# Kernel optimization log

Measured on AMD Instinct MI355X. Metric: run time of the kernel, lower is better.

## Reference

```python
import jax, jax.numpy as jnp
import numpy as np

E, T_MAX, H, L, V = 384, 256, 6, 6, 65
DH = E // H  # 64
EPS = 1e-5


def setup_inputs() -> dict:
    key = jax.random.key(0)
    ks = jax.random.split(key, 24)
    B, T = 128, 256
    s = 0.02
    inp = {
        "input_indices": jax.random.randint(ks[0], (B, T), 0, V, dtype=jnp.int64) if jax.config.read("jax_enable_x64") else jax.random.randint(ks[0], (B, T), 0, V, dtype=jnp.int32),
        "targets": jax.random.randint(ks[1], (B, T), 0, V, dtype=jnp.int32),
        "tok_emb": s * jax.random.normal(ks[2], (V, E), jnp.float32),
        "pos_emb": s * jax.random.normal(ks[3], (T_MAX, E), jnp.float32),
        "Wq": s * jax.random.normal(ks[4], (L, H, E, DH), jnp.float32),
        "Wk": s * jax.random.normal(ks[5], (L, H, E, DH), jnp.float32),
        "Wv": s * jax.random.normal(ks[6], (L, H, E, DH), jnp.float32),
        "Wo": s * jax.random.normal(ks[7], (L, E, E), jnp.float32),
        "bo": jnp.zeros((L, E), jnp.float32),
        "ln1_s": jnp.ones((L, E), jnp.float32),
        "ln1_b": jnp.zeros((L, E), jnp.float32),
        "ln2_s": jnp.ones((L, E), jnp.float32),
        "ln2_b": jnp.zeros((L, E), jnp.float32),
        "W1": s * jax.random.normal(ks[8], (L, E, 4 * E), jnp.float32),
        "b1": jnp.zeros((L, 4 * E), jnp.float32),
        "W2": s * jax.random.normal(ks[9], (L, 4 * E, E), jnp.float32),
        "b2": jnp.zeros((L, E), jnp.float32),
        "lnf_s": jnp.ones((E,), jnp.float32),
        "lnf_b": jnp.zeros((E,), jnp.float32),
        "Wout": s * jax.random.normal(ks[10], (E, V), jnp.float32),
        "bout": jnp.zeros((V,), jnp.float32),
    }
    return inp


def _ln(x, s, b):
    m = x.mean(-1, keepdims=True)
    v = ((x - m) ** 2).mean(-1, keepdims=True)
    return (x - m) * jax.lax.rsqrt(v + EPS) * s + b


def _forward(input_indices, targets, tok_emb, pos_emb, Wq, Wk, Wv, Wo, bo,
             ln1_s, ln1_b, ln2_s, ln2_b, W1, b1, W2, b2, lnf_s, lnf_b, Wout, bout):
    B, T = input_indices.shape
    x = tok_emb[input_indices] + pos_emb[:T]  # [B,T,E]
    causal = jnp.tril(jnp.ones((T, T), bool))
    scale = DH ** -0.5

    def block(x, p):
        wq, wk, wv, wo, bo_, l1s, l1b, l2s, l2b, w1, b1_, w2, b2_ = p
        h = _ln(x, l1s, l1b)
        q = jnp.einsum("bte,hed->bhtd", h, wq)
        k = jnp.einsum("bte,hed->bhtd", h, wk)
        v = jnp.einsum("bte,hed->bhtd", h, wv)
        scores = jnp.einsum("bhtd,bhsd->bhts", q, k) * scale
        scores = jnp.where(causal, scores, -jnp.inf)
        w = jax.nn.softmax(scores, axis=-1)
        att = jnp.einsum("bhts,bhsd->bhtd", w, v)  # [B,H,T,DH]
        att = att.transpose(0, 2, 1, 3).reshape(B, T, E)  # concat heads
        x = x + att @ wo + bo_
        h2 = _ln(x, l2s, l2b)
        ff = jax.nn.relu(h2 @ w1 + b1_) @ w2 + b2_
        return x + ff, None

    x, _ = jax.lax.scan(block, x, (Wq, Wk, Wv, Wo, bo, ln1_s, ln1_b, ln2_s, ln2_b, W1, b1, W2, b2))
    x = _ln(x, lnf_s, lnf_b)
    logits = x @ Wout + bout  # [B,T,V]
    logp = jax.nn.log_softmax(logits, axis=-1)
    nll = -jnp.take_along_axis(logp, targets[..., None], axis=-1)[..., 0]
    loss = nll.mean()
    return logits, loss


def reference(input_indices, targets, tok_emb, pos_emb, Wq, Wk, Wv, Wo, bo,
              ln1_s, ln1_b, ln2_s, ln2_b, W1, b1, W2, b2, lnf_s, lnf_b, Wout, bout):
    return _forward(input_indices, targets, tok_emb, pos_emb, Wq, Wk, Wv, Wo, bo,
                    ln1_s, ln1_b, ln2_s, ln2_b, W1, b1, W2, b2, lnf_s, lnf_b, Wout, bout)
```

## Files before the change

### kernel.cpp

```cpp
#include <hip/hip_runtime.h>

#define BT      32768
#define T_SEQ   256
#define E_DIM   384
#define NH      6
#define NL      6
#define VOC     65
#define FF_DIM  1536
#define QKV_N   1152

typedef short bf16x8 __attribute__((ext_vector_type(8)));
typedef float f32x4  __attribute__((ext_vector_type(4)));
typedef unsigned short u16;

typedef const unsigned int __attribute__((address_space(1))) gu32;
typedef unsigned int       __attribute__((address_space(3))) lu32;

__device__ __forceinline__ u16 f2bf(float x) {
  unsigned u = __builtin_bit_cast(unsigned, x);
  u += 0x7fffu + ((u >> 16) & 1u);
  return (u16)(u >> 16);
}
__device__ __forceinline__ float bf2f(u16 v) {
  unsigned u = ((unsigned)v) << 16;
  return __builtin_bit_cast(float, u);
}

__device__ __forceinline__ void load_lds_16(const void* g, void* l) {
  __builtin_amdgcn_global_load_lds((gu32*)g, (lu32*)l, 16, 0, 0);
}

__global__ __launch_bounds__(256) void transpose_t(
    const float* __restrict__ src, u16* __restrict__ dst, int R, int C,
    long sbs, long dbs_outer, int inner, long dbs_inner, long dbase) {
  __shared__ float t[32][33];
  const int b = blockIdx.z;
  const float* s = src + (long)b * sbs;
  u16* d = dst + dbase + (long)(b / inner) * dbs_outer + (long)(b % inner) * dbs_inner;
  const int r0 = blockIdx.x * 32, c0 = blockIdx.y * 32;
  const int tx = threadIdx.x & 31, ty = threadIdx.x >> 5;
#pragma unroll
  for (int i = 0; i < 4; i++) {
    int rr = ty + i * 8;
    int r = r0 + rr, c = c0 + tx;
    if (r < R && c < C) t[rr][tx] = s[(long)r * C + c];
  }
  __syncthreads();
#pragma unroll
  for (int i = 0; i < 4; i++) {
    int cc = ty + i * 8;
    int c = c0 + cc, r = r0 + tx;
    if (c < C && r < R) d[(long)c * R + r] = f2bf(t[tx][cc]);
  }
}

__global__ __launch_bounds__(256) void embed_k(const int* __restrict__ idx,
                                               const float* __restrict__ tok,
                                               const float* __restrict__ pos,
                                               u16* __restrict__ x) {
  int i = blockIdx.x * 256 + threadIdx.x;
  int bt = i / 48, q = i - bt * 48;
  int t = bt & 255;
  const float4* tp = (const float4*)(tok + (size_t)idx[bt] * E_DIM + q * 8);
  const float4* pp = (const float4*)(pos + (size_t)t * E_DIM + q * 8);
  float4 a0 = tp[0], a1 = tp[1], p0 = pp[0], p1 = pp[1];
  u16 o[8];
  o[0] = f2bf(a0.x + p0.x); o[1] = f2bf(a0.y + p0.y);
  o[2] = f2bf(a0.z + p0.z); o[3] = f2bf(a0.w + p0.w);
  o[4] = f2bf(a1.x + p1.x); o[5] = f2bf(a1.y + p1.y);
  o[6] = f2bf(a1.z + p1.z); o[7] = f2bf(a1.w + p1.w);
  *(bf16x8*)(x + (size_t)bt * E_DIM + q * 8) = *(bf16x8*)o;
}

__global__ __launch_bounds__(256) void ln_k(const u16* __restrict__ x,
                                            const float* __restrict__ gam,
                                            const float* __restrict__ bet,
                                            u16* __restrict__ out) {
  int tid = threadIdx.x, lane = tid & 63, w = tid >> 6;
  size_t token = (size_t)blockIdx.x * 4 + w;
  const u16* xr = x + token * E_DIM;
  u16 raw[6];
  *(uint2*)raw          = *(const uint2*)(xr + 4 * lane);
  *(unsigned*)(raw + 4) = *(const unsigned*)(xr + 256 + 2 * lane);
  float v[6]; float s = 0.f;
#pragma unroll
  for (int i = 0; i < 6; i++) { v[i] = bf2f(raw[i]); s += v[i]; }
#pragma unroll
  for (int d = 1; d < 64; d <<= 1) s += __shfl_xor(s, d);
  float mean = s * (1.f / E_DIM);
  float q = 0.f;
#pragma unroll
  for (int i = 0; i < 6; i++) { float d0 = v[i] - mean; q += d0 * d0; }
#pragma unroll
  for (int d = 1; d < 64; d <<= 1) q += __shfl_xor(q, d);
  float r = rsqrtf(q * (1.f / E_DIM) + 1e-5f);
  int e[6] = {4 * lane, 4 * lane + 1, 4 * lane + 2, 4 * lane + 3,
              256 + 2 * lane, 256 + 2 * lane + 1};
  u16 o[6];
#pragma unroll
  for (int i = 0; i < 6; i++)
    o[i] = f2bf((v[i] - mean) * r * gam[e[i]] + bet[e[i]]);
  u16* orow = out + token * E_DIM;
  *(uint2*)(orow + 4 * lane)        = *(uint2*)o;
  *(unsigned*)(orow + 256 + 2 * lane) = *(unsigned*)(o + 4);
}

__global__ __launch_bounds__(256) void gemm_bt(
    const u16* __restrict__ A, const u16* __restrict__ Bt, int K, int Nstore,
    const float* __restrict__ bias, const u16* __restrict__ resid,
    u16* __restrict__ outH, float* __restrict__ outF, int relu) {
  __shared__ u16 smem[8192];
  u16* As = smem;
  u16* Bs = smem + 4096;
  const int tid = threadIdx.x, lane = tid & 63, wv = tid >> 6;
  const int quad = lane >> 4, l16 = lane & 15;
  const int m0 = blockIdx.x * 128, n0 = blockIdx.y * 128;
  const int wm = (wv & 1) * 64, wn = (wv >> 1) * 64;
  const int srow = lane >> 2, scol = (lane & 3) * 8;

  f32x4 acc[4][4];
#pragma unroll
  for (int i = 0; i < 4; i++)
#pragma unroll
    for (int j = 0; j < 4; j++) acc[i][j] = (f32x4){0.f, 0.f, 0.f, 0.f};

  for (int k0 = 0; k0 < K; k0 += 32) {
    __syncthreads();
#pragma unroll
    for (int j = 0; j < 2; j++) {
      int rid = wv * 2 + j;
      int r = rid * 16 + srow;
      load_lds_16(A  + (size_t)(m0 + r) * K + (k0 + scol), &As[rid * 512]);
      load_lds_16(Bt + (size_t)(n0 + r) * K + (k0 + scol), &Bs[rid * 512]);
    }
    __syncthreads();
    bf16x8 af[4], bfr[4];
#pragma unroll
    for (int i = 0; i < 4; i++) af[i]  = *(const bf16x8*)&As[(wm + i * 16 + l16) * 32 + quad * 8];
#pragma unroll
    for (int j = 0; j < 4; j++) bfr[j] = *(const bf16x8*)&Bs[(wn + j * 16 + l16) * 32 + quad * 8];
#pragma unroll
    for (int i = 0; i < 4; i++)
#pragma unroll
      for (int j = 0; j < 4; j++)
        acc[i][j] = __builtin_amdgcn_mfma_f32_16x16x32_bf16(af[i], bfr[j], acc[i][j], 0, 0, 0);
  }

  if (outH) {
#pragma unroll
    for (int p = 0; p < 4; p++) {
      __syncthreads();
      if ((wv >> 1) == (p >> 1)) {
#pragma unroll
        for (int jj = 0; jj < 2; jj++) {
          int j = (p & 1) * 2 + jj;
          int gn = n0 + wn + j * 16 + l16;
          float bv = bias ? bias[gn] : 0.f;
          int lcol = jj * 16 + l16;
#pragma unroll
          for (int i = 0; i < 4; i++)
#pragma unroll
            for (int r = 0; r < 4; r++) {
              float v = acc[i][j][r] + bv;
              if (relu) v = fmaxf(v, 0.f);
              smem[(wm + i * 16 + quad * 4 + r) * 36 + lcol] = f2bf(v);
            }
        }
      }
      __syncthreads();
      const int gc0 = n0 + p * 32;
#pragma unroll
      for (int s = 0; s < 4; s++) {
        int row = s * 32 + (tid >> 3);
        int seg = (tid & 7) * 4;
        u16 pk[4];
        *(uint2*)pk = *(const uint2*)&smem[row * 36 + seg];
        size_t o = (size_t)(m0 + row) * Nstore + gc0 + seg;
        if (resid) {
          u16 rv[4];
          *(uint2*)rv = *(const uint2*)&resid[o];
#pragma unroll
          for (int q2 = 0; q2 < 4; q2++) pk[q2] = f2bf(bf2f(pk[q2]) + bf2f(rv[q2]));
        }
        *(uint2*)&outH[o] = *(uint2*)pk;
      }
    }
  } else {
#pragma unroll
    for (int j = 0; j < 4; j++) {
      const int gn = n0 + wn + j * 16 + l16;
      if (gn < Nstore) {
        const float bv = bias ? bias[gn] : 0.f;
#pragma unroll
        for (int i = 0; i < 4; i++)
#pragma unroll
          for (int r = 0; r < 4; r++) {
            const int gm = m0 + wm + i * 16 + quad * 4 + r;
            outF[(size_t)gm * Nstore + gn] = acc[i][j][r] + bv;
          }
      }
    }
  }
}

__global__ __launch_bounds__(512) void attn_k(const u16* __restrict__ qkv,
                                              u16* __restrict__ att) {
  __shared__ u16 Kc[64 * 64];
  __shared__ u16 Vtc[64 * 64];
  __shared__ u16 Pl[8 * 32 * 64];
  const int b = blockIdx.x / NH, h = blockIdx.x % NH;
  const int tid = threadIdx.x, lane = tid & 63, w = tid >> 6;
  const int quad = lane >> 4, l16 = lane & 15;
  const int rowb = b * T_SEQ;

  bf16x8 qf[2][2];
#pragma unroll
  for (int mi = 0; mi < 2; mi++)
#pragma unroll
    for (int kk = 0; kk < 2; kk++)
      qf[mi][kk] = *(const bf16x8*)(qkv + (size_t)(rowb + w * 32 + mi * 16 + l16) * QKV_N +
                                    h * 64 + kk * 32 + quad * 8);

  f32x4 Oa[2][4];
  float mrun[2][4], lrun[2][4];
#pragma unroll
  for (int mi = 0; mi < 2; mi++) {
#pragma unroll
    for (int di = 0; di < 4; di++) Oa[mi][di] = (f32x4){0.f, 0.f, 0.f, 0.f};
#pragma unroll
    for (int r = 0; r < 4; r++) { mrun[mi][r] = -1e30f; lrun[mi][r] = 0.f; }
  }

  u16* Pw = &Pl[w * 2048];
  const int nch = (w >> 1) + 1;
  const int sr = tid >> 3, sseg = (tid & 7) * 8;

  for (int c = 0; c < 4; c++) {
    const int s0 = c * 64;
    __syncthreads();
    *(uint4*)&Kc[sr * 64 + sseg] =
        *(const uint4*)(qkv + (size_t)(rowb + s0 + sr) * QKV_N + 384 + h * 64 + sseg);
    {
      union { uint4 u; u16 us[8]; } tb;
      tb.u = *(const uint4*)(qkv + (size_t)(rowb + s0 + sr) * QKV_N + 768 + h * 64 + sseg);
#pragma unroll
      for (int j = 0; j < 8; j++) Vtc[(sseg + j) * 64 + sr] = tb.us[j];
    }
    __syncthreads();
    if (c >= nch) continue;

    f32x4 S[2][4];
    bf16x8 kf[4][2];
#pragma unroll
    for (int ni = 0; ni < 4; ni++)
#pragma unroll
      for (int kk = 0; kk < 2; kk++)
        kf[ni][kk] = *(const bf16x8*)&Kc[(ni * 16 + l16) * 64 + kk * 32 + quad * 8];
#pragma unroll
    for (int mi = 0; mi < 2; mi++)
#pragma unroll
      for (int ni = 0; ni < 4; ni++) {
        f32x4 z = (f32x4){0.f, 0.f, 0.f, 0.f};
        z = __builtin_amdgcn_mfma_f32_16x16x32_bf16(qf[mi][0], kf[ni][0], z, 0, 0, 0);
        S[mi][ni] = __builtin_amdgcn_mfma_f32_16x16x32_bf16(qf[mi][1], kf[ni][1], z, 0, 0, 0);
      }
    const bool diag = (c == nch - 1);
#pragma unroll
    for (int mi = 0; mi < 2; mi++)
#pragma unroll
      for (int ni = 0; ni < 4; ni++)
#pragma unroll
        for (int r = 0; r < 4; r++) {
          float xv = S[mi][ni][r] * 0.125f;
          if (diag) {
            int t = w * 32 + mi * 16 + quad * 4 + r;
            int s = s0 + ni * 16 + l16;
            if (s > t) xv = -1e30f;
          }
          S[mi][ni][r] = xv;
        }
#pragma unroll
    for (int mi = 0; mi < 2; mi++)
#pragma unroll
      for (int r = 0; r < 4; r++) {
        float mx = fmaxf(fmaxf(S[mi][0][r], S[mi][1][r]), fmaxf(S[mi][2][r], S[mi][3][r]));
        mx = fmaxf(mx, __shfl_xor(mx, 1));
        mx = fmaxf(mx, __shfl_xor(mx, 2));
        mx = fmaxf(mx, __shfl_xor(mx, 4));
        mx = fmaxf(mx, __shfl_xor(mx, 8));
        float mnew = fmaxf(mrun[mi][r], mx);
        float alpha = __expf(mrun[mi][r] - mnew);
        float ls = 0.f;
#pragma unroll
        for (int ni = 0; ni < 4; ni++) {
          float p = __expf(S[mi][ni][r] - mnew);
          S[mi][ni][r] = p; ls += p;
        }
        ls += __shfl_xor(ls, 1); ls += __shfl_xor(ls, 2);
        ls += __shfl_xor(ls, 4); ls += __shfl_xor(ls, 8);
        lrun[mi][r] = lrun[mi][r] * alpha + ls;
        mrun[mi][r] = mnew;
#pragma unroll
        for (int di = 0; di < 4; di++) Oa[mi][di][r] *= alpha;
      }
#pragma unroll
    for (int mi = 0; mi < 2; mi++)
#pragma unroll
      for (int ni = 0; ni < 4; ni++)
#pragma unroll
        for (int r = 0; r < 4; r++)
          Pw[(mi * 16 + quad * 4 + r) * 64 + ni * 16 + l16] = f2bf(S[mi][ni][r]);
    bf16x8 pf[2][2], vf[4][2];
#pragma unroll
    for (int mi = 0; mi < 2; mi++)
#pragma unroll
      for (int kk = 0; kk < 2; kk++)
        pf[mi][kk] = *(const bf16x8*)&Pw[(mi * 16 + l16) * 64 + kk * 32 + quad * 8];
#pragma unroll
    for (int di = 0; di < 4; di++)
#pragma unroll
      for (int kk = 0; kk < 2; kk++)
        vf[di][kk] = *(const bf16x8*)&Vtc[(di * 16 + l16) * 64 + kk * 32 + quad * 8];
#pragma unroll
    for (int mi = 0; mi < 2; mi++)
#pragma unroll
      for (int di = 0; di < 4; di++) {
        Oa[mi][di] = __builtin_amdgcn_mfma_f32_16x16x32_bf16(pf[mi][0], vf[di][0], Oa[mi][di], 0, 0, 0);
        Oa[mi][di] = __builtin_amdgcn_mfma_f32_16x16x32_bf16(pf[mi][1], vf[di][1], Oa[mi][di], 0, 0, 0);
      }
  }

#pragma unroll
  for (int mi = 0; mi < 2; mi++)
#pragma unroll
    for (int r = 0; r < 4; r++) {
      float inv = 1.f / lrun[mi][r];
      int t = w * 32 + mi * 16 + quad * 4 + r;
#pragma unroll
      for (int di = 0; di < 4; di++)
        att[(size_t)(rowb + t) * E_DIM + h * 64 + di * 16 + l16] = f2bf(Oa[mi][di][r] * inv);
    }
}

__global__ __launch_bounds__(256) void loss_k(const float* __restrict__ logits,
                                              const int* __restrict__ tgt,
                                              float* __restrict__ loss) {
  __shared__ float part[4];
  const int tid = threadIdx.x, lane = tid & 63, w = tid >> 6;
  const int wave_id = blockIdx.x * 4 + w;
  float acc = 0.f;
  for (int t = wave_id; t < BT; t += 2048) {
    const float* row = logits + (size_t)t * VOC;
    float a = row[lane];
    float b = (lane == 0) ? row[64] : -1e30f;
    float mx = fmaxf(a, b);
#pragma unroll
    for (int d = 1; d < 64; d <<= 1) mx = fmaxf(mx, __shfl_xor(mx, d));
    float sum = __expf(a - mx) + ((lane == 0) ? __expf(b - mx) : 0.f);
#pragma unroll
    for (int d = 1; d < 64; d <<= 1) sum += __shfl_xor(sum, d);
    if (lane == 0) acc += mx + __logf(sum) - row[tgt[t]];
  }
  if (lane == 0) part[w] = acc;
  __syncthreads();
  if (tid == 0)
    atomicAdd(loss, (part[0] + part[1] + part[2] + part[3]) * (1.f / (float)BT));
}

extern "C" void kernel_launch(void* const* d_in, const int* in_sizes, int n_in,
                              void* d_out, int out_size, void* d_ws, size_t ws_size,
                              hipStream_t stream) {
  (void)in_sizes; (void)n_in; (void)out_size; (void)ws_size;
  const int*   idx  = (const int*)d_in[0];
  const int*   tgt  = (const int*)d_in[1];
  const float* tok  = (const float*)d_in[2];
  const float* pos  = (const float*)d_in[3];
  const float* Wq   = (const float*)d_in[4];
  const float* Wk   = (const float*)d_in[5];
  const float* Wv   = (const float*)d_in[6];
  const float* Wo   = (const float*)d_in[7];
  const float* bo   = (const float*)d_in[8];
  const float* ln1s = (const float*)d_in[9];
  const float* ln1b = (const float*)d_in[10];
  const float* ln2s = (const float*)d_in[11];
  const float* ln2b = (const float*)d_in[12];
  const float* W1   = (const float*)d_in[13];
  const float* b1   = (const float*)d_in[14];
  const float* W2   = (const float*)d_in[15];
  const float* b2   = (const float*)d_in[16];
  const float* lnfs = (const float*)d_in[17];
  const float* lnfb = (const float*)d_in[18];
  const float* Wout = (const float*)d_in[19];
  const float* bout = (const float*)d_in[20];

  char* w = (char*)d_ws;
  u16* x      = (u16*)w;    w += (size_t)BT * E_DIM * 2;
  u16* hb     = (u16*)w;    w += (size_t)BT * E_DIM * 2;
  u16* attb   = (u16*)w;    w += (size_t)BT * E_DIM * 2;
  u16* big    = (u16*)w;    w += (size_t)BT * FF_DIM * 2;
  u16* Wqkv_t = (u16*)w;    w += (size_t)NL * QKV_N * E_DIM * 2;
  u16* Wo_t   = (u16*)w;    w += (size_t)NL * E_DIM * E_DIM * 2;
  u16* W1_t   = (u16*)w;    w += (size_t)NL * FF_DIM * E_DIM * 2;
  u16* W2_t   = (u16*)w;    w += (size_t)NL * E_DIM * FF_DIM * 2;
  u16* Wout_t = (u16*)w;    w += (size_t)128 * E_DIM * 2;
  u16* qkv = big;
  u16* ff  = big;

  float* logits = (float*)d_out;
  float* loss   = logits + (size_t)BT * VOC;

  hipMemsetAsync(Wout_t, 0, 128 * E_DIM * 2, stream);
  transpose_t<<<dim3(12, 2, 36), 256, 0, stream>>>(Wq, Wqkv_t, 384, 64,
      24576, 442368, 6, 24576, 0);
  transpose_t<<<dim3(12, 2, 36), 256, 0, stream>>>(Wk, Wqkv_t, 384, 64,
      24576, 442368, 6, 24576, (long)384 * 384);
  transpose_t<<<dim3(12, 2, 36), 256, 0, stream>>>(Wv, Wqkv_t, 384, 64,
      24576, 442368, 6, 24576, (long)768 * 384);
  transpose_t<<<dim3(12, 12, 6), 256, 0, stream>>>(Wo, Wo_t, 384, 384,
      147456, 147456, 1, 0, 0);
  transpose_t<<<dim3(12, 48, 6), 256, 0, stream>>>(W1, W1_t, 384, 1536,
      589824, 589824, 1, 0, 0);
  transpose_t<<<dim3(48, 12, 6), 256, 0, stream>>>(W2, W2_t, 1536, 384,
      589824, 589824, 1, 0, 0);
  transpose_t<<<dim3(12, 3, 1), 256, 0, stream>>>(Wout, Wout_t, 384, 65,
      0, 0, 1, 0, 0);

  embed_k<<<6144, 256, 0, stream>>>(idx, tok, pos, x);

  for (int l = 0; l < NL; l++) {
    ln_k<<<8192, 256, 0, stream>>>(x, ln1s + l * E_DIM, ln1b + l * E_DIM, hb);
    gemm_bt<<<dim3(256, 9), 256, 0, stream>>>(hb, Wqkv_t + (size_t)l * QKV_N * E_DIM,
                                              384, QKV_N, nullptr, nullptr, qkv, nullptr, 0);
    attn_k<<<768, 512, 0, stream>>>(qkv, attb);
    gemm_bt<<<dim3(256, 3), 256, 0, stream>>>(attb, Wo_t + (size_t)l * E_DIM * E_DIM,
                                              384, E_DIM, bo + l * E_DIM, x, x, nullptr, 0);
    ln_k<<<8192, 256, 0, stream>>>(x, ln2s + l * E_DIM, ln2b + l * E_DIM, hb);
    gemm_bt<<<dim3(256, 12), 256, 0, stream>>>(hb, W1_t + (size_t)l * FF_DIM * E_DIM,
                                               384, FF_DIM, b1 + l * FF_DIM, nullptr, ff, nullptr, 1);
    gemm_bt<<<dim3(256, 3), 256, 0, stream>>>(ff, W2_t + (size_t)l * E_DIM * FF_DIM,
                                              1536, E_DIM, b2 + l * E_DIM, x, x, nullptr, 0);
  }
  ln_k<<<8192, 256, 0, stream>>>(x, lnfs, lnfb, hb);
  gemm_bt<<<dim3(256, 1), 256, 0, stream>>>(hb, Wout_t, 384, VOC, bout, nullptr, nullptr, logits, 0);

  hipMemsetAsync(loss, 0, 4, stream);
  loss_k<<<512, 256, 0, stream>>>(logits, tgt, loss);
}
```

Before: 1.912 ms.

## Double-buffer GEMM LDS tiles and use 256-row tiles for wide GEMMs

The GEMM kernel becomes a template on the M tile size and double-buffers its A/B LDS tiles, so the global-to-LDS load for the next K step is issued before the MFMAs on the current step. This removes one of the two barriers per K iteration. The QKV and FF1 GEMMs switch to 256-row tiles, which halves the number of blocks and gives more reuse of each B tile. The cost is more LDS (up to 48 KB) and more accumulator registers per block, and launch bounds are set to keep 2-3 blocks per CU.

```diff
diff --git a/kernel.cpp b/kernel.cpp
--- a/kernel.cpp
+++ b/kernel.cpp
@@ -101,55 +101,73 @@
   for (int i = 0; i < 6; i++)
     o[i] = f2bf((v[i] - mean) * r * gam[e[i]] + bet[e[i]]);
   u16* orow = out + token * E_DIM;
-  *(uint2*)(orow + 4 * lane)        = *(uint2*)o;
+  *(uint2*)(orow + 4 * lane)          = *(uint2*)o;
   *(unsigned*)(orow + 256 + 2 * lane) = *(unsigned*)(o + 4);
 }
 
-__global__ __launch_bounds__(256) void gemm_bt(
+template<int TM>
+__global__ __launch_bounds__(256, TM == 256 ? 2 : 3) void gemm_bt(
     const u16* __restrict__ A, const u16* __restrict__ Bt, int K, int Nstore,
     const float* __restrict__ bias, const u16* __restrict__ resid,
     u16* __restrict__ outH, float* __restrict__ outF, int relu) {
-  __shared__ u16 smem[8192];
+  constexpr int MI = TM / 32;
+  __shared__ u16 smem[TM * 64 + 8192];
   u16* As = smem;
-  u16* Bs = smem + 4096;
+  u16* Bs = smem + TM * 64;
   const int tid = threadIdx.x, lane = tid & 63, wv = tid >> 6;
   const int quad = lane >> 4, l16 = lane & 15;
-  const int m0 = blockIdx.x * 128, n0 = blockIdx.y * 128;
-  const int wm = (wv & 1) * 64, wn = (wv >> 1) * 64;
+  const int m0 = blockIdx.x * TM, n0 = blockIdx.y * 128;
+  const int wm = (wv & 1) * (TM / 2), wn = (wv >> 1) * 64;
   const int srow = lane >> 2, scol = (lane & 3) * 8;
 
-  f32x4 acc[4][4];
-#pragma unroll
-  for (int i = 0; i < 4; i++)
+  f32x4 acc[MI][4];
+#pragma unroll
+  for (int i = 0; i < MI; i++)
 #pragma unroll
     for (int j = 0; j < 4; j++) acc[i][j] = (f32x4){0.f, 0.f, 0.f, 0.f};
 
-  for (int k0 = 0; k0 < K; k0 += 32) {
-    __syncthreads();
+  auto stage = [&](int sel, int k0) {
+    u16* Ab = As + sel * (TM * 32);
+    u16* Bb = Bs + sel * 4096;
+#pragma unroll
+    for (int j = 0; j < TM / 64; j++) {
+      int rid = wv * (TM / 64) + j;
+      int r = rid * 16 + srow;
+      load_lds_16(A + (size_t)(m0 + r) * K + (k0 + scol), Ab + rid * 512);
+    }
 #pragma unroll
     for (int j = 0; j < 2; j++) {
       int rid = wv * 2 + j;
       int r = rid * 16 + srow;
-      load_lds_16(A  + (size_t)(m0 + r) * K + (k0 + scol), &As[rid * 512]);
-      load_lds_16(Bt + (size_t)(n0 + r) * K + (k0 + scol), &Bs[rid * 512]);
-    }
-    __syncthreads();
-    bf16x8 af[4], bfr[4];
-#pragma unroll
-    for (int i = 0; i < 4; i++) af[i]  = *(const bf16x8*)&As[(wm + i * 16 + l16) * 32 + quad * 8];
-#pragma unroll
-    for (int j = 0; j < 4; j++) bfr[j] = *(const bf16x8*)&Bs[(wn + j * 16 + l16) * 32 + quad * 8];
-#pragma unroll
-    for (int i = 0; i < 4; i++)
+      load_lds_16(Bt + (size_t)(n0 + r) * K + (k0 + scol), Bb + rid * 512);
+    }
+  };
+
+  const int NK = K >> 5;
+  stage(0, 0);
+  __syncthreads();
+  for (int kt = 0; kt < NK; kt++) {
+    const int cur = kt & 1;
+    if (kt + 1 < NK) stage(cur ^ 1, (kt + 1) * 32);
+    const u16* Ab = As + cur * (TM * 32);
+    const u16* Bb = Bs + cur * 4096;
+    bf16x8 af[MI], bfr[4];
+#pragma unroll
+    for (int i = 0; i < MI; i++) af[i]  = *(const bf16x8*)&Ab[(wm + i * 16 + l16) * 32 + quad * 8];
+#pragma unroll
+    for (int j = 0; j < 4; j++)  bfr[j] = *(const bf16x8*)&Bb[(wn + j * 16 + l16) * 32 + quad * 8];
+#pragma unroll
+    for (int i = 0; i < MI; i++)
 #pragma unroll
       for (int j = 0; j < 4; j++)
         acc[i][j] = __builtin_amdgcn_mfma_f32_16x16x32_bf16(af[i], bfr[j], acc[i][j], 0, 0, 0);
+    __syncthreads();
   }
 
   if (outH) {
 #pragma unroll
     for (int p = 0; p < 4; p++) {
-      __syncthreads();
+      if (p) __syncthreads();
       if ((wv >> 1) == (p >> 1)) {
 #pragma unroll
         for (int jj = 0; jj < 2; jj++) {
@@ -158,7 +176,7 @@
           float bv = bias ? bias[gn] : 0.f;
           int lcol = jj * 16 + l16;
 #pragma unroll
-          for (int i = 0; i < 4; i++)
+          for (int i = 0; i < MI; i++)
 #pragma unroll
             for (int r = 0; r < 4; r++) {
               float v = acc[i][j][r] + bv;
@@ -170,7 +188,7 @@
       __syncthreads();
       const int gc0 = n0 + p * 32;
 #pragma unroll
-      for (int s = 0; s < 4; s++) {
+      for (int s = 0; s < TM / 32; s++) {
         int row = s * 32 + (tid >> 3);
         int seg = (tid & 7) * 4;
         u16 pk[4];
@@ -192,7 +210,7 @@
       if (gn < Nstore) {
         const float bv = bias ? bias[gn] : 0.f;
 #pragma unroll
-        for (int i = 0; i < 4; i++)
+        for (int i = 0; i < MI; i++)
 #pragma unroll
           for (int r = 0; r < 4; r++) {
             const int gm = m0 + wm + i * 16 + quad * 4 + r;
@@ -429,19 +447,19 @@
 
   for (int l = 0; l < NL; l++) {
     ln_k<<<8192, 256, 0, stream>>>(x, ln1s + l * E_DIM, ln1b + l * E_DIM, hb);
-    gemm_bt<<<dim3(256, 9), 256, 0, stream>>>(hb, Wqkv_t + (size_t)l * QKV_N * E_DIM,
-                                              384, QKV_N, nullptr, nullptr, qkv, nullptr, 0);
+    gemm_bt<256><<<dim3(128, 9), 256, 0, stream>>>(hb, Wqkv_t + (size_t)l * QKV_N * E_DIM,
+                                                   384, QKV_N, nullptr, nullptr, qkv, nullptr, 0);
     attn_k<<<768, 512, 0, stream>>>(qkv, attb);
-    gemm_bt<<<dim3(256, 3), 256, 0, stream>>>(attb, Wo_t + (size_t)l * E_DIM * E_DIM,
-                                              384, E_DIM, bo + l * E_DIM, x, x, nullptr, 0);
+    gemm_bt<128><<<dim3(256, 3), 256, 0, stream>>>(attb, Wo_t + (size_t)l * E_DIM * E_DIM,
+                                                   384, E_DIM, bo + l * E_DIM, x, x, nullptr, 0);
     ln_k<<<8192, 256, 0, stream>>>(x, ln2s + l * E_DIM, ln2b + l * E_DIM, hb);
-    gemm_bt<<<dim3(256, 12), 256, 0, stream>>>(hb, W1_t + (size_t)l * FF_DIM * E_DIM,
-                                               384, FF_DIM, b1 + l * FF_DIM, nullptr, ff, nullptr, 1);
-    gemm_bt<<<dim3(256, 3), 256, 0, stream>>>(ff, W2_t + (size_t)l * E_DIM * FF_DIM,
-                                              1536, E_DIM, b2 + l * E_DIM, x, x, nullptr, 0);
+    gemm_bt<256><<<dim3(128, 12), 256, 0, stream>>>(hb, W1_t + (size_t)l * FF_DIM * E_DIM,
+                                                    384, FF_DIM, b1 + l * FF_DIM, nullptr, ff, nullptr, 1);
+    gemm_bt<128><<<dim3(256, 3), 256, 0, stream>>>(ff, W2_t + (size_t)l * E_DIM * FF_DIM,
+                                                   1536, E_DIM, b2 + l * E_DIM, x, x, nullptr, 0);
   }
   ln_k<<<8192, 256, 0, stream>>>(x, lnfs, lnfb, hb);
-  gemm_bt<<<dim3(256, 1), 256, 0, stream>>>(hb, Wout_t, 384, VOC, bout, nullptr, nullptr, logits, 0);
+  gemm_bt<128><<<dim3(256, 1), 256, 0, stream>>>(hb, Wout_t, 384, VOC, bout, nullptr, nullptr, logits, 0);
 
   hipMemsetAsync(loss, 0, 4, stream);
   loss_k<<<512, 256, 0, stream>>>(logits, tgt, loss);
```

Measured after the change: 1.866 ms. 1.02x faster.

## Load GEMM operands directly from global into registers with double buffering

Applied to the files above, without the earlier changes.

Replaces the shared-memory staged GEMM, which used global_load_lds with two barriers per K-step, by a version where each wave loads its MFMA fragments straight from global memory into registers. Two register buffers hold alternating K-halves so loads overlap the MFMAs. The epilogue becomes per-wave, using a private LDS tile with 16-byte stores and no block-wide barriers. This removes cross-wave data sharing, so each wave refetches A and B rows through cache. The fragment-shaped global loads are also less coalesced.

```diff
diff --git a/kernel.cpp b/kernel.cpp
--- a/kernel.cpp
+++ b/kernel.cpp
@@ -13,9 +13,6 @@
 typedef float f32x4  __attribute__((ext_vector_type(4)));
 typedef unsigned short u16;
 
-typedef const unsigned int __attribute__((address_space(1))) gu32;
-typedef unsigned int       __attribute__((address_space(3))) lu32;
-
 __device__ __forceinline__ u16 f2bf(float x) {
   unsigned u = __builtin_bit_cast(unsigned, x);
   u += 0x7fffu + ((u >> 16) & 1u);
@@ -24,10 +21,6 @@
 __device__ __forceinline__ float bf2f(u16 v) {
   unsigned u = ((unsigned)v) << 16;
   return __builtin_bit_cast(float, u);
-}
-
-__device__ __forceinline__ void load_lds_16(const void* g, void* l) {
-  __builtin_amdgcn_global_load_lds((gu32*)g, (lu32*)l, 16, 0, 0);
 }
 
 __global__ __launch_bounds__(256) void transpose_t(
@@ -101,22 +94,21 @@
   for (int i = 0; i < 6; i++)
     o[i] = f2bf((v[i] - mean) * r * gam[e[i]] + bet[e[i]]);
   u16* orow = out + token * E_DIM;
-  *(uint2*)(orow + 4 * lane)        = *(uint2*)o;
+  *(uint2*)(orow + 4 * lane)          = *(uint2*)o;
   *(unsigned*)(orow + 256 + 2 * lane) = *(unsigned*)(o + 4);
 }
 
-__global__ __launch_bounds__(256) void gemm_bt(
+__global__ __launch_bounds__(256) void gemm_nb(
     const u16* __restrict__ A, const u16* __restrict__ Bt, int K, int Nstore,
     const float* __restrict__ bias, const u16* __restrict__ resid,
     u16* __restrict__ outH, float* __restrict__ outF, int relu) {
-  __shared__ u16 smem[8192];
-  u16* As = smem;
-  u16* Bs = smem + 4096;
+  __shared__ u16 cb[4][64 * 68];
   const int tid = threadIdx.x, lane = tid & 63, wv = tid >> 6;
   const int quad = lane >> 4, l16 = lane & 15;
-  const int m0 = blockIdx.x * 128, n0 = blockIdx.y * 128;
-  const int wm = (wv & 1) * 64, wn = (wv >> 1) * 64;
-  const int srow = lane >> 2, scol = (lane & 3) * 8;
+  const int m0 = blockIdx.x * 128 + (wv & 1) * 64;
+  const int n0 = blockIdx.y * 128 + (wv >> 1) * 64;
+  const u16* Ap = A  + (size_t)(m0 + l16) * K + quad * 8;
+  const u16* Bp = Bt + (size_t)(n0 + l16) * K + quad * 8;
 
   f32x4 acc[4][4];
 #pragma unroll
@@ -124,78 +116,76 @@
 #pragma unroll
     for (int j = 0; j < 4; j++) acc[i][j] = (f32x4){0.f, 0.f, 0.f, 0.f};
 
-  for (int k0 = 0; k0 < K; k0 += 32) {
-    __syncthreads();
-#pragma unroll
-    for (int j = 0; j < 2; j++) {
-      int rid = wv * 2 + j;
-      int r = rid * 16 + srow;
-      load_lds_16(A  + (size_t)(m0 + r) * K + (k0 + scol), &As[rid * 512]);
-      load_lds_16(Bt + (size_t)(n0 + r) * K + (k0 + scol), &Bs[rid * 512]);
-    }
-    __syncthreads();
-    bf16x8 af[4], bfr[4];
-#pragma unroll
-    for (int i = 0; i < 4; i++) af[i]  = *(const bf16x8*)&As[(wm + i * 16 + l16) * 32 + quad * 8];
-#pragma unroll
-    for (int j = 0; j < 4; j++) bfr[j] = *(const bf16x8*)&Bs[(wn + j * 16 + l16) * 32 + quad * 8];
+  bf16x8 a0[4], b0[4], a1[4], b1[4];
+#pragma unroll
+  for (int i = 0; i < 4; i++) a0[i] = *(const bf16x8*)(Ap + (size_t)(i * 16) * K);
+#pragma unroll
+  for (int j = 0; j < 4; j++) b0[j] = *(const bf16x8*)(Bp + (size_t)(j * 16) * K);
+
+  for (int k0 = 0; k0 < K; k0 += 64) {
+#pragma unroll
+    for (int i = 0; i < 4; i++) a1[i] = *(const bf16x8*)(Ap + (size_t)(i * 16) * K + k0 + 32);
+#pragma unroll
+    for (int j = 0; j < 4; j++) b1[j] = *(const bf16x8*)(Bp + (size_t)(j * 16) * K + k0 + 32);
 #pragma unroll
     for (int i = 0; i < 4; i++)
 #pragma unroll
       for (int j = 0; j < 4; j++)
-        acc[i][j] = __builtin_amdgcn_mfma_f32_16x16x32_bf16(af[i], bfr[j], acc[i][j], 0, 0, 0);
+        acc[i][j] = __builtin_amdgcn_mfma_f32_16x16x32_bf16(a0[i], b0[j], acc[i][j], 0, 0, 0);
+    if (k0 + 64 < K) {
+#pragma unroll
+      for (int i = 0; i < 4; i++) a0[i] = *(const bf16x8*)(Ap + (size_t)(i * 16) * K + k0 + 64);
+#pragma unroll
+      for (int j = 0; j < 4; j++) b0[j] = *(const bf16x8*)(Bp + (size_t)(j * 16) * K + k0 + 64);
+    }
+#pragma unroll
+    for (int i = 0; i < 4; i++)
+#pragma unroll
+      for (int j = 0; j < 4; j++)
+        acc[i][j] = __builtin_amdgcn_mfma_f32_16x16x32_bf16(a1[i], b1[j], acc[i][j], 0, 0, 0);
   }
 
   if (outH) {
-#pragma unroll
-    for (int p = 0; p < 4; p++) {
-      __syncthreads();
-      if ((wv >> 1) == (p >> 1)) {
-#pragma unroll
-        for (int jj = 0; jj < 2; jj++) {
-          int j = (p & 1) * 2 + jj;
-          int gn = n0 + wn + j * 16 + l16;
-          float bv = bias ? bias[gn] : 0.f;
-          int lcol = jj * 16 + l16;
-#pragma unroll
-          for (int i = 0; i < 4; i++)
-#pragma unroll
-            for (int r = 0; r < 4; r++) {
-              float v = acc[i][j][r] + bv;
-              if (relu) v = fmaxf(v, 0.f);
-              smem[(wm + i * 16 + quad * 4 + r) * 36 + lcol] = f2bf(v);
-            }
+    u16* L = cb[wv];
+#pragma unroll
+    for (int j = 0; j < 4; j++) {
+      int gn = n0 + j * 16 + l16;
+      float bv = bias ? bias[gn] : 0.f;
+#pragma unroll
+      for (int i = 0; i < 4; i++)
+#pragma unroll
+        for (int r = 0; r < 4; r++) {
+          float v = acc[i][j][r] + bv;
+          if (relu) v = fmaxf(v, 0.f);
+          L[(i * 16 + quad * 4 + r) * 68 + j * 16 + l16] = f2bf(v);
         }
+    }
+    const int sr = lane >> 3, seg = (lane & 7) * 8;
+#pragma unroll
+    for (int s = 0; s < 8; s++) {
+      int row = s * 8 + sr;
+      u16 pk[8];
+      *(uint4*)pk = *(const uint4*)&L[row * 68 + seg];
+      size_t o = (size_t)(m0 + row) * Nstore + n0 + seg;
+      if (resid) {
+        u16 rv[8];
+        *(uint4*)rv = *(const uint4*)&resid[o];
+#pragma unroll
+        for (int q2 = 0; q2 < 8; q2++) pk[q2] = f2bf(bf2f(pk[q2]) + bf2f(rv[q2]));
       }
-      __syncthreads();
-      const int gc0 = n0 + p * 32;
-#pragma unroll
-      for (int s = 0; s < 4; s++) {
-        int row = s * 32 + (tid >> 3);
-        int seg = (tid & 7) * 4;
-        u16 pk[4];
-        *(uint2*)pk = *(const uint2*)&smem[row * 36 + seg];
-        size_t o = (size_t)(m0 + row) * Nstore + gc0 + seg;
-        if (resid) {
-          u16 rv[4];
-          *(uint2*)rv = *(const uint2*)&resid[o];
-#pragma unroll
-          for (int q2 = 0; q2 < 4; q2++) pk[q2] = f2bf(bf2f(pk[q2]) + bf2f(rv[q2]));
-        }
-        *(uint2*)&outH[o] = *(uint2*)pk;
-      }
+      *(uint4*)&outH[o] = *(uint4*)pk;
     }
   } else {
 #pragma unroll
     for (int j = 0; j < 4; j++) {
-      const int gn = n0 + wn + j * 16 + l16;
+      const int gn = n0 + j * 16 + l16;
       if (gn < Nstore) {
         const float bv = bias ? bias[gn] : 0.f;
 #pragma unroll
         for (int i = 0; i < 4; i++)
 #pragma unroll
           for (int r = 0; r < 4; r++) {
-            const int gm = m0 + wm + i * 16 + quad * 4 + r;
+            const int gm = m0 + i * 16 + quad * 4 + r;
             outF[(size_t)gm * Nstore + gn] = acc[i][j][r] + bv;
           }
       }
@@ -429,19 +419,19 @@
 
   for (int l = 0; l < NL; l++) {
     ln_k<<<8192, 256, 0, stream>>>(x, ln1s + l * E_DIM, ln1b + l * E_DIM, hb);
-    gemm_bt<<<dim3(256, 9), 256, 0, stream>>>(hb, Wqkv_t + (size_t)l * QKV_N * E_DIM,
+    gemm_nb<<<dim3(256, 9), 256, 0, stream>>>(hb, Wqkv_t + (size_t)l * QKV_N * E_DIM,
                                               384, QKV_N, nullptr, nullptr, qkv, nullptr, 0);
     attn_k<<<768, 512, 0, stream>>>(qkv, attb);
-    gemm_bt<<<dim3(256, 3), 256, 0, stream>>>(attb, Wo_t + (size_t)l * E_DIM * E_DIM,
+    gemm_nb<<<dim3(256, 3), 256, 0, stream>>>(attb, Wo_t + (size_t)l * E_DIM * E_DIM,
                                               384, E_DIM, bo + l * E_DIM, x, x, nullptr, 0);
     ln_k<<<8192, 256, 0, stream>>>(x, ln2s + l * E_DIM, ln2b + l * E_DIM, hb);
-    gemm_bt<<<dim3(256, 12), 256, 0, stream>>>(hb, W1_t + (size_t)l * FF_DIM * E_DIM,
+    gemm_nb<<<dim3(256, 12), 256, 0, stream>>>(hb, W1_t + (size_t)l * FF_DIM * E_DIM,
                                                384, FF_DIM, b1 + l * FF_DIM, nullptr, ff, nullptr, 1);
-    gemm_bt<<<dim3(256, 3), 256, 0, stream>>>(ff, W2_t + (size_t)l * E_DIM * FF_DIM,
+    gemm_nb<<<dim3(256, 3), 256, 0, stream>>>(ff, W2_t + (size_t)l * E_DIM * FF_DIM,
                                               1536, E_DIM, b2 + l * E_DIM, x, x, nullptr, 0);
   }
   ln_k<<<8192, 256, 0, stream>>>(x, lnfs, lnfb, hb);
-  gemm_bt<<<dim3(256, 1), 256, 0, stream>>>(hb, Wout_t, 384, VOC, bout, nullptr, nullptr, logits, 0);
+  gemm_nb<<<dim3(256, 1), 256, 0, stream>>>(hb, Wout_t, 384, VOC, bout, nullptr, nullptr, logits, 0);
 
   hipMemsetAsync(loss, 0, 4, stream);
   loss_k<<<512, 256, 0, stream>>>(logits, tgt, loss);
```

Result: slower. 3.087 ms (+61.4%).

## Double-buffer GEMM tiles via register prefetch with padded LDS rows

Applied to the files above, without the earlier changes.

Replaces the direct global-to-LDS loads in the GEMM with register-staged prefetching two k-tiles ahead into double-buffered shared memory, using a single barrier per iteration. LDS rows are padded to 34 elements to reduce bank conflicts on fragment reads. The aim is to overlap global memory latency with MFMA work and remove one barrier per k-step. In exchange it uses more registers and twice the LDS, which may lower occupancy, and the 34-element stride leaves the 16-byte vector accesses only 4-byte aligned.

```diff
diff --git a/kernel.cpp b/kernel.cpp
--- a/kernel.cpp
+++ b/kernel.cpp
@@ -13,9 +13,6 @@
 typedef float f32x4  __attribute__((ext_vector_type(4)));
 typedef unsigned short u16;
 
-typedef const unsigned int __attribute__((address_space(1))) gu32;
-typedef unsigned int       __attribute__((address_space(3))) lu32;
-
 __device__ __forceinline__ u16 f2bf(float x) {
   unsigned u = __builtin_bit_cast(unsigned, x);
   u += 0x7fffu + ((u >> 16) & 1u);
@@ -26,8 +23,8 @@
   return __builtin_bit_cast(float, u);
 }
 
-__device__ __forceinline__ void load_lds_16(const void* g, void* l) {
-  __builtin_amdgcn_global_load_lds((gu32*)g, (lu32*)l, 16, 0, 0);
+__device__ __forceinline__ void lds_barrier() {
+  asm volatile("s_waitcnt lgkmcnt(0)\n\ts_barrier" ::: "memory");
 }
 
 __global__ __launch_bounds__(256) void transpose_t(
@@ -101,22 +98,27 @@
   for (int i = 0; i < 6; i++)
     o[i] = f2bf((v[i] - mean) * r * gam[e[i]] + bet[e[i]]);
   u16* orow = out + token * E_DIM;
-  *(uint2*)(orow + 4 * lane)        = *(uint2*)o;
+  *(uint2*)(orow + 4 * lane)          = *(uint2*)o;
   *(unsigned*)(orow + 256 + 2 * lane) = *(unsigned*)(o + 4);
 }
 
-__global__ __launch_bounds__(256) void gemm_bt(
+__global__ __launch_bounds__(256) void gemm_p(
     const u16* __restrict__ A, const u16* __restrict__ Bt, int K, int Nstore,
     const float* __restrict__ bias, const u16* __restrict__ resid,
     u16* __restrict__ outH, float* __restrict__ outF, int relu) {
-  __shared__ u16 smem[8192];
-  u16* As = smem;
-  u16* Bs = smem + 4096;
+  __shared__ u16 smem[17408];
   const int tid = threadIdx.x, lane = tid & 63, wv = tid >> 6;
   const int quad = lane >> 4, l16 = lane & 15;
   const int m0 = blockIdx.x * 128, n0 = blockIdx.y * 128;
   const int wm = (wv & 1) * 64, wn = (wv >> 1) * 64;
-  const int srow = lane >> 2, scol = (lane & 3) * 8;
+
+  const int srow0 = tid >> 2, scol = (tid & 3) * 8;
+  const int srow1 = srow0 + 64;
+  const u16* ApG0 = A  + (size_t)(m0 + srow0) * K + scol;
+  const u16* ApG1 = A  + (size_t)(m0 + srow1) * K + scol;
+  const u16* BpG0 = Bt + (size_t)(n0 + srow0) * K + scol;
+  const u16* BpG1 = Bt + (size_t)(n0 + srow1) * K + scol;
+  const int wofs0 = srow0 * 34 + scol, wofs1 = srow1 * 34 + scol;
 
   f32x4 acc[4][4];
 #pragma unroll
@@ -124,32 +126,48 @@
 #pragma unroll
     for (int j = 0; j < 4; j++) acc[i][j] = (f32x4){0.f, 0.f, 0.f, 0.f};
 
-  for (int k0 = 0; k0 < K; k0 += 32) {
-    __syncthreads();
-#pragma unroll
-    for (int j = 0; j < 2; j++) {
-      int rid = wv * 2 + j;
-      int r = rid * 16 + srow;
-      load_lds_16(A  + (size_t)(m0 + r) * K + (k0 + scol), &As[rid * 512]);
-      load_lds_16(Bt + (size_t)(n0 + r) * K + (k0 + scol), &Bs[rid * 512]);
-    }
-    __syncthreads();
+  uint4 ra0, ra1, rb0, rb1;
+  ra0 = *(const uint4*)ApG0; ra1 = *(const uint4*)ApG1;
+  rb0 = *(const uint4*)BpG0; rb1 = *(const uint4*)BpG1;
+  *(uint4*)&smem[wofs0] = ra0; *(uint4*)&smem[wofs1] = ra1;
+  *(uint4*)&smem[8704 + wofs0] = rb0; *(uint4*)&smem[8704 + wofs1] = rb1;
+  ra0 = *(const uint4*)(ApG0 + 32); ra1 = *(const uint4*)(ApG1 + 32);
+  rb0 = *(const uint4*)(BpG0 + 32); rb1 = *(const uint4*)(BpG1 + 32);
+  lds_barrier();
+
+  const int NK = K >> 5;
+  for (int kt = 0; kt < NK; kt++) {
+    const int cur = kt & 1, nxt = cur ^ 1;
+    if (kt + 1 < NK) {
+      *(uint4*)&smem[nxt * 4352 + wofs0] = ra0;
+      *(uint4*)&smem[nxt * 4352 + wofs1] = ra1;
+      *(uint4*)&smem[8704 + nxt * 4352 + wofs0] = rb0;
+      *(uint4*)&smem[8704 + nxt * 4352 + wofs1] = rb1;
+    }
+    if (kt + 2 < NK) {
+      const int k2 = (kt + 2) * 32;
+      ra0 = *(const uint4*)(ApG0 + k2); ra1 = *(const uint4*)(ApG1 + k2);
+      rb0 = *(const uint4*)(BpG0 + k2); rb1 = *(const uint4*)(BpG1 + k2);
+    }
+    const u16* Ab = smem + cur * 4352;
+    const u16* Bb = smem + 8704 + cur * 4352;
     bf16x8 af[4], bfr[4];
 #pragma unroll
-    for (int i = 0; i < 4; i++) af[i]  = *(const bf16x8*)&As[(wm + i * 16 + l16) * 32 + quad * 8];
-#pragma unroll
-    for (int j = 0; j < 4; j++) bfr[j] = *(const bf16x8*)&Bs[(wn + j * 16 + l16) * 32 + quad * 8];
+    for (int i = 0; i < 4; i++) af[i]  = *(const bf16x8*)&Ab[(wm + i * 16 + l16) * 34 + quad * 8];
+#pragma unroll
+    for (int j = 0; j < 4; j++) bfr[j] = *(const bf16x8*)&Bb[(wn + j * 16 + l16) * 34 + quad * 8];
 #pragma unroll
     for (int i = 0; i < 4; i++)
 #pragma unroll
       for (int j = 0; j < 4; j++)
         acc[i][j] = __builtin_amdgcn_mfma_f32_16x16x32_bf16(af[i], bfr[j], acc[i][j], 0, 0, 0);
+    lds_barrier();
   }
 
   if (outH) {
 #pragma unroll
     for (int p = 0; p < 4; p++) {
-      __syncthreads();
+      if (p) __syncthreads();
       if ((wv >> 1) == (p >> 1)) {
 #pragma unroll
         for (int jj = 0; jj < 2; jj++) {
@@ -429,19 +447,19 @@
 
   for (int l = 0; l < NL; l++) {
     ln_k<<<8192, 256, 0, stream>>>(x, ln1s + l * E_DIM, ln1b + l * E_DIM, hb);
-    gemm_bt<<<dim3(256, 9), 256, 0, stream>>>(hb, Wqkv_t + (size_t)l * QKV_N * E_DIM,
-                                              384, QKV_N, nullptr, nullptr, qkv, nullptr, 0);
+    gemm_p<<<dim3(256, 9), 256, 0, stream>>>(hb, Wqkv_t + (size_t)l * QKV_N * E_DIM,
+                                             384, QKV_N, nullptr, nullptr, qkv, nullptr, 0);
     attn_k<<<768, 512, 0, stream>>>(qkv, attb);
-    gemm_bt<<<dim3(256, 3), 256, 0, stream>>>(attb, Wo_t + (size_t)l * E_DIM * E_DIM,
-                                              384, E_DIM, bo + l * E_DIM, x, x, nullptr, 0);
+    gemm_p<<<dim3(256, 3), 256, 0, stream>>>(attb, Wo_t + (size_t)l * E_DIM * E_DIM,
+                                             384, E_DIM, bo + l * E_DIM, x, x, nullptr, 0);
     ln_k<<<8192, 256, 0, stream>>>(x, ln2s + l * E_DIM, ln2b + l * E_DIM, hb);
-    gemm_bt<<<dim3(256, 12), 256, 0, stream>>>(hb, W1_t + (size_t)l * FF_DIM * E_DIM,
-                                               384, FF_DIM, b1 + l * FF_DIM, nullptr, ff, nullptr, 1);
-    gemm_bt<<<dim3(256, 3), 256, 0, stream>>>(ff, W2_t + (size_t)l * E_DIM * FF_DIM,
-                                              1536, E_DIM, b2 + l * E_DIM, x, x, nullptr, 0);
+    gemm_p<<<dim3(256, 12), 256, 0, stream>>>(hb, W1_t + (size_t)l * FF_DIM * E_DIM,
+                                              384, FF_DIM, b1 + l * FF_DIM, nullptr, ff, nullptr, 1);
+    gemm_p<<<dim3(256, 3), 256, 0, stream>>>(ff, W2_t + (size_t)l * E_DIM * FF_DIM,
+                                             1536, E_DIM, b2 + l * E_DIM, x, x, nullptr, 0);
   }
   ln_k<<<8192, 256, 0, stream>>>(x, lnfs, lnfb, hb);
-  gemm_bt<<<dim3(256, 1), 256, 0, stream>>>(hb, Wout_t, 384, VOC, bout, nullptr, nullptr, logits, 0);
+  gemm_p<<<dim3(256, 1), 256, 0, stream>>>(hb, Wout_t, 384, VOC, bout, nullptr, nullptr, logits, 0);
 
   hipMemsetAsync(loss, 0, 4, stream);
   loss_k<<<512, 256, 0, stream>>>(logits, tgt, loss);
```

Result: slower. 3.519 ms (+84.0%).
